# Optimization experiments

Measured on AMD Instinct MI355X. Metric: run time of the kernel, lower is better.

## Reference

```python
import jax, jax.numpy as jnp
import numpy as np

K = 3       # kernel_size
STRIDE = 1
PAD = 1
EPS = 1e-12  # F.normalize eps


def setup_inputs() -> dict:
    key = jax.random.key(0)
    k1, k2, k3 = jax.random.split(key, 3)
    x = jax.random.normal(k1, (8, 128, 112, 112), dtype=jnp.float32)
    weight = jax.random.normal(k2, (256, 128, K, K), dtype=jnp.float32)
    bias = jax.random.normal(k3, (256,), dtype=jnp.float32)
    return {"x": x, "weight": weight, "bias": bias}


def reference(x, weight, bias):
    B, C, H, W = x.shape
    Cout = weight.shape[0]
    oh = (H + 2 * PAD - K) // STRIDE + 1
    ow = (W + 2 * PAD - K) // STRIDE + 1
    # im2col: [B, C*K*K, oh, ow]; feature order (C, kh, kw), same as torch F.unfold
    patches = jax.lax.conv_general_dilated_patches(
        x, (K, K), (STRIDE, STRIDE), [(PAD, PAD), (PAD, PAD)],
        dimension_numbers=("NCHW", "OIHW", "NCHW"))
    u = patches.reshape(B, C * K * K, oh * ow)
    # L2-normalize each patch column (dim=1), matching F.normalize(p=2, dim=1)
    norm = jnp.sqrt(jnp.sum(u * u, axis=1, keepdims=True))
    u = u / jnp.maximum(norm, EPS)
    # GEMM: [Cout, C*K*K] x [B, C*K*K, L] -> [B, Cout, L]
    out = jnp.einsum("od,bdl->bol", weight.reshape(Cout, -1), u)
    out = out.reshape(B, Cout, oh, ow) + bias[None, :, None, None]
    return out
```

## Files before the change

### kernel.cpp

```cpp
#include <hip/hip_runtime.h>

#define CIN    128
#define COUT   256
#define Hh     112
#define Ww     112
#define HW     12544
#define NBATCH 8
#define NPIX   (NBATCH*HW)
#define KD     (CIN*9)
#define PH     114
#define PPIX   (NBATCH*PH*PH)

typedef __bf16         v8bf __attribute__((ext_vector_type(8)));
typedef float          v4f  __attribute__((ext_vector_type(4)));
typedef unsigned short v8us __attribute__((ext_vector_type(8)));

__device__ __forceinline__ unsigned short f2bf(float f) {
  unsigned int u = __float_as_uint(f);
  u += 0x7FFFu + ((u >> 16) & 1u);
  return (unsigned short)(u >> 16);
}

__device__ __forceinline__ void gl_lds16(const void* g, void* l) {
  __builtin_amdgcn_global_load_lds(
      (const __attribute__((address_space(1))) void*)g,
      (__attribute__((address_space(3))) void*)l, 16, 0, 0);
}

__global__ __launch_bounds__(256) void k_sq_convert(
    const float* __restrict__ x, unsigned short* __restrict__ xbp,
    float* __restrict__ sq2)
{
  int gid  = blockIdx.x * 256 + threadIdx.x;
  int half = gid >= NPIX ? 1 : 0;
  int p    = gid - half * NPIX;
  int b  = p / HW;
  int hw = p - b * HW;
  int oy = hw / Ww;
  int ox = hw - oy * Ww;
  const float* xp = x + (size_t)b * CIN * HW + hw + (size_t)half * 64 * HW;
  unsigned short* xo = xbp + ((size_t)(b * PH + oy + 1) * PH + (ox + 1)) * CIN + half * 64;
  float acc = 0.0f;
  for (int c0 = 0; c0 < 64; c0 += 8) {
    v8us buf;
#pragma unroll
    for (int j = 0; j < 8; ++j) {
      float v = xp[(size_t)(c0 + j) * HW];
      acc += v * v;
      buf[j] = f2bf(v);
    }
    *(v8us*)(xo + c0) = buf;
  }
  sq2[(size_t)half * NPIX + p] = acc;
}

__global__ __launch_bounds__(256) void k_zero_border(unsigned short* __restrict__ xbp)
{
  int gid = blockIdx.x * 256 + threadIdx.x;
  if (gid >= PPIX) return;
  int b  = gid / (PH * PH);
  int r  = gid - b * PH * PH;
  int py = r / PH;
  int px = r - py * PH;
  if (py != 0 && py != PH - 1 && px != 0 && px != PH - 1) return;
  unsigned short* dst = xbp + (size_t)gid * CIN;
  v8us z;
#pragma unroll
  for (int j = 0; j < 8; ++j) z[j] = 0;
#pragma unroll
  for (int c0 = 0; c0 < CIN; c0 += 8) *(v8us*)(dst + c0) = z;
}

__global__ __launch_bounds__(256) void k_invnorm(
    const float* __restrict__ sq2, float* __restrict__ invn)
{
  int p = blockIdx.x * 256 + threadIdx.x;
  if (p >= NPIX) return;
  int b  = p / HW;  int r  = p - b * HW;
  int oy = r / Ww;  int ox = r - oy * Ww;
  float acc = 0.0f;
#pragma unroll
  for (int dy = -1; dy <= 1; ++dy) {
    int iy = oy + dy;
    if (iy < 0 || iy >= Hh) continue;
#pragma unroll
    for (int dx = -1; dx <= 1; ++dx) {
      int ix = ox + dx;
      if (ix < 0 || ix >= Ww) continue;
      int q = b * HW + iy * Ww + ix;
      acc += sq2[q] + sq2[NPIX + q];
    }
  }
  invn[p] = 1.0f / fmaxf(sqrtf(acc), 1e-12f);
}

__global__ __launch_bounds__(256) void k_packw(
    const float* __restrict__ w, unsigned short* __restrict__ wp)
{
  int idx = blockIdx.x * 256 + threadIdx.x;
  int o  = idx / KD;
  int rr = idx - o * KD;
  int kk = rr >> 7;
  int c  = rr & 127;
  wp[idx] = f2bf(w[(size_t)o * KD + c * 9 + kk]);
}

__global__ __launch_bounds__(256, 3) void k_conv(
    const unsigned short* __restrict__ wp,
    const unsigned short* __restrict__ xbp,
    const float* __restrict__ invn,
    const float* __restrict__ bias,
    float* __restrict__ out)
{
  __shared__ unsigned short As[128 * 64];
  __shared__ unsigned short Bs[128 * 64];

  int tid  = threadIdx.x;
  int lane = tid & 63;
  int wid  = tid >> 6;
  int wm   = wid >> 1, wn = wid & 1;
  int quad = lane >> 4;
  int l16  = lane & 15;

  int bn = blockIdx.x;
  int bm = blockIdx.y;

  int srow = tid >> 3;
  int g    = (tid & 7) ^ (srow & 7);

  const unsigned short* asrc = wp + (size_t)(bm * 128 + srow) * KD + g * 8;

  int pb[4];
#pragma unroll
  for (int j = 0; j < 4; ++j) {
    int n  = bn * 128 + j * 32 + srow;
    int b  = n / HW;  int r  = n - b * HW;
    int oy = r / Ww;  int ox = r - oy * Ww;
    pb[j] = ((b * PH + oy) * PH + ox) * CIN + g * 8;
  }

  v4f acc[4][4];
#pragma unroll
  for (int mt = 0; mt < 4; ++mt)
#pragma unroll
    for (int nt = 0; nt < 4; ++nt)
#pragma unroll
      for (int j = 0; j < 4; ++j) acc[mt][nt][j] = 0.0f;

  const int khs[9] = {0,0,0,1,1,1,2,2,2};
  const int kws[9] = {0,1,2,0,1,2,0,1,2};

  for (int s = 0; s < 18; ++s) {
    int kk   = s >> 1;
    int c0   = (s & 1) * 64;
    int soff = (khs[kk] * PH + kws[kk]) * CIN + c0;

#pragma unroll
    for (int j = 0; j < 4; ++j)
      gl_lds16(asrc + (size_t)j * 32 * KD + s * 64,
               &As[(wid * 8 + j * 32) * 64]);
#pragma unroll
    for (int j = 0; j < 4; ++j)
      gl_lds16(xbp + pb[j] + soff,
               &Bs[(wid * 8 + j * 32) * 64]);

    __syncthreads();

#pragma unroll
    for (int h = 0; h < 2; ++h) {
      v8bf af[4], bf[4];
      int cch = (h * 4 + quad) ^ (l16 & 7);
#pragma unroll
      for (int mt = 0; mt < 4; ++mt) {
        int m = wm * 64 + mt * 16 + l16;
        af[mt] = *(const v8bf*)&As[m * 64 + cch * 8];
      }
#pragma unroll
      for (int nt = 0; nt < 4; ++nt) {
        int nr = wn * 64 + nt * 16 + l16;
        bf[nt] = *(const v8bf*)&Bs[nr * 64 + cch * 8];
      }
#pragma unroll
      for (int mt = 0; mt < 4; ++mt)
#pragma unroll
        for (int nt = 0; nt < 4; ++nt)
          acc[mt][nt] = __builtin_amdgcn_mfma_f32_16x16x32_bf16(
              af[mt], bf[nt], acc[mt][nt], 0, 0, 0);
    }

    __syncthreads();
  }

#pragma unroll
  for (int nt = 0; nt < 4; ++nt) {
    int n = bn * 128 + wn * 64 + nt * 16 + l16;
    float inv = invn[n];
    int b = n / HW;  int r = n - b * HW;
    float* op = out + (size_t)b * COUT * HW + r;
#pragma unroll
    for (int mt = 0; mt < 4; ++mt) {
      int o0 = bm * 128 + wm * 64 + mt * 16 + quad * 4;
#pragma unroll
      for (int reg = 0; reg < 4; ++reg) {
        int o = o0 + reg;
        op[(size_t)o * HW] = acc[mt][nt][reg] * inv + bias[o];
      }
    }
  }
}

extern "C" void kernel_launch(void* const* d_in, const int* in_sizes, int n_in,
                              void* d_out, int out_size, void* d_ws, size_t ws_size,
                              hipStream_t stream) {
  const float* x    = (const float*)d_in[0];
  const float* w    = (const float*)d_in[1];
  const float* bias = (const float*)d_in[2];
  float* out        = (float*)d_out;

  char* ws = (char*)d_ws;
  unsigned short* xbp = (unsigned short*)ws;
  size_t off = (size_t)PPIX * CIN * 2;
  unsigned short* wpk = (unsigned short*)(ws + off);
  off += (size_t)COUT * KD * 2;
  float* sq2 = (float*)(ws + off);
  off += (size_t)2 * NPIX * 4;
  float* invn = (float*)(ws + off);

  k_sq_convert<<<2 * NPIX / 256, 256, 0, stream>>>(x, xbp, sq2);
  k_zero_border<<<(PPIX + 255) / 256, 256, 0, stream>>>(xbp);
  k_packw<<<(COUT * KD) / 256, 256, 0, stream>>>(w, wpk);
  k_invnorm<<<NPIX / 256, 256, 0, stream>>>(sq2, invn);
  k_conv<<<dim3(NPIX / 128, COUT / 128), 256, 0, stream>>>(wpk, xbp, invn, bias, out);
}
```

Baseline: 244.4 us.

## Transpose input via LDS, stage conv epilogue through LDS, and swizzle block order

```diff
diff --git a/kernel.cpp b/kernel.cpp
--- a/kernel.cpp
+++ b/kernel.cpp
@@ -13,7 +13,6 @@
 
 typedef __bf16         v8bf __attribute__((ext_vector_type(8)));
 typedef float          v4f  __attribute__((ext_vector_type(4)));
-typedef unsigned short v8us __attribute__((ext_vector_type(8)));
 
 __device__ __forceinline__ unsigned short f2bf(float f) {
   unsigned int u = __float_as_uint(f);
@@ -27,31 +26,57 @@
       (__attribute__((address_space(3))) void*)l, 16, 0, 0);
 }
 
+#define SQS 65
 __global__ __launch_bounds__(256) void k_sq_convert(
     const float* __restrict__ x, unsigned short* __restrict__ xbp,
-    float* __restrict__ sq2)
-{
-  int gid  = blockIdx.x * 256 + threadIdx.x;
-  int half = gid >= NPIX ? 1 : 0;
-  int p    = gid - half * NPIX;
-  int b  = p / HW;
-  int hw = p - b * HW;
-  int oy = hw / Ww;
-  int ox = hw - oy * Ww;
-  const float* xp = x + (size_t)b * CIN * HW + hw + (size_t)half * 64 * HW;
-  unsigned short* xo = xbp + ((size_t)(b * PH + oy + 1) * PH + (ox + 1)) * CIN + half * 64;
+    float* __restrict__ sq)
+{
+  __shared__ unsigned int US[56 * SQS];
+  __shared__ float sqp[56 * 4];
+
+  int tid = threadIdx.x;
+  int l   = tid & 63;
+  int wid = tid >> 6;
+  int bid = blockIdx.x;
+  int xh  = bid & 1;
+  int t2  = bid >> 1;
+  int b   = t2 / Hh;
+  int oy  = t2 - b * Hh;
+  int ox0 = xh * 56;
+
+  const float* xp = x + (size_t)b * CIN * HW + oy * Ww + ox0;
+  bool valid = l < 56;
   float acc = 0.0f;
-  for (int c0 = 0; c0 < 64; c0 += 8) {
-    v8us buf;
-#pragma unroll
-    for (int j = 0; j < 8; ++j) {
-      float v = xp[(size_t)(c0 + j) * HW];
-      acc += v * v;
-      buf[j] = f2bf(v);
-    }
-    *(v8us*)(xo + c0) = buf;
-  }
-  sq2[(size_t)half * NPIX + p] = acc;
+#pragma unroll
+  for (int it = 0; it < 16; ++it) {
+    int cp = it * 4 + wid;
+    int c0 = cp * 2;
+    float v0 = 0.0f, v1 = 0.0f;
+    if (valid) {
+      v0 = xp[(size_t)c0 * HW + l];
+      v1 = xp[(size_t)(c0 + 1) * HW + l];
+    }
+    acc += v0 * v0 + v1 * v1;
+    unsigned int pk = (unsigned int)f2bf(v0) | ((unsigned int)f2bf(v1) << 16);
+    if (valid) US[l * SQS + cp] = pk;
+  }
+  if (valid) sqp[l * 4 + wid] = acc;
+  __syncthreads();
+
+  if (tid < 56) {
+    float s = sqp[tid * 4] + sqp[tid * 4 + 1] + sqp[tid * 4 + 2] + sqp[tid * 4 + 3];
+    sq[(size_t)b * HW + oy * Ww + ox0 + tid] = s;
+  }
+
+  unsigned int* dst = (unsigned int*)xbp +
+      ((size_t)(b * PH + oy + 1) * PH + (ox0 + 1)) * (CIN / 2);
+  for (int h = tid; h < 896; h += 256) {
+    int u0  = h * 4;
+    int pix = u0 >> 6, cu = u0 & 63;
+    const unsigned int* s = &US[pix * SQS + cu];
+    uint4 vv; vv.x = s[0]; vv.y = s[1]; vv.z = s[2]; vv.w = s[3];
+    *(uint4*)(dst + u0) = vv;
+  }
 }
 
 __global__ __launch_bounds__(256) void k_zero_border(unsigned short* __restrict__ xbp)
@@ -63,21 +88,20 @@
   int py = r / PH;
   int px = r - py * PH;
   if (py != 0 && py != PH - 1 && px != 0 && px != PH - 1) return;
-  unsigned short* dst = xbp + (size_t)gid * CIN;
-  v8us z;
-#pragma unroll
-  for (int j = 0; j < 8; ++j) z[j] = 0;
-#pragma unroll
-  for (int c0 = 0; c0 < CIN; c0 += 8) *(v8us*)(dst + c0) = z;
+  unsigned int* dst = (unsigned int*)xbp + (size_t)gid * (CIN / 2);
+  uint4 z = {0, 0, 0, 0};
+#pragma unroll
+  for (int c0 = 0; c0 < 64; c0 += 4) *(uint4*)(dst + c0) = z;
 }
 
 __global__ __launch_bounds__(256) void k_invnorm(
-    const float* __restrict__ sq2, float* __restrict__ invn)
+    const float* __restrict__ sq, float* __restrict__ invn)
 {
   int p = blockIdx.x * 256 + threadIdx.x;
   if (p >= NPIX) return;
   int b  = p / HW;  int r  = p - b * HW;
   int oy = r / Ww;  int ox = r - oy * Ww;
+  const float* s = sq + (size_t)b * HW;
   float acc = 0.0f;
 #pragma unroll
   for (int dy = -1; dy <= 1; ++dy) {
@@ -87,8 +111,7 @@
     for (int dx = -1; dx <= 1; ++dx) {
       int ix = ox + dx;
       if (ix < 0 || ix >= Ww) continue;
-      int q = b * HW + iy * Ww + ix;
-      acc += sq2[q] + sq2[NPIX + q];
+      acc += s[iy * Ww + ix];
     }
   }
   invn[p] = 1.0f / fmaxf(sqrtf(acc), 1e-12f);
@@ -105,6 +128,7 @@
   wp[idx] = f2bf(w[(size_t)o * KD + c * 9 + kk]);
 }
 
+#define SLAB_S 132
 __global__ __launch_bounds__(256, 3) void k_conv(
     const unsigned short* __restrict__ wp,
     const unsigned short* __restrict__ xbp,
@@ -112,8 +136,10 @@
     const float* __restrict__ bias,
     float* __restrict__ out)
 {
-  __shared__ unsigned short As[128 * 64];
-  __shared__ unsigned short Bs[128 * 64];
+  __shared__ __align__(16) char smem[64 * SLAB_S * 4];
+  unsigned short* As = (unsigned short*)smem;
+  unsigned short* Bs = As + 128 * 64;
+  float* slab = (float*)smem;
 
   int tid  = threadIdx.x;
   int lane = tid & 63;
@@ -122,21 +148,24 @@
   int quad = lane >> 4;
   int l16  = lane & 15;
 
-  int bn = blockIdx.x;
-  int bm = blockIdx.y;
+  int L  = blockIdx.x;
+  int g  = L >> 4;
+  int j  = L & 15;
+  int bn = g * 8 + (j & 7);
+  int bm = j >> 3;
 
   int srow = tid >> 3;
-  int g    = (tid & 7) ^ (srow & 7);
-
-  const unsigned short* asrc = wp + (size_t)(bm * 128 + srow) * KD + g * 8;
+  int g16  = (tid & 7) ^ (srow & 7);
+
+  const unsigned short* asrc = wp + (size_t)(bm * 128 + srow) * KD + g16 * 8;
 
   int pb[4];
 #pragma unroll
-  for (int j = 0; j < 4; ++j) {
-    int n  = bn * 128 + j * 32 + srow;
+  for (int jj = 0; jj < 4; ++jj) {
+    int n  = bn * 128 + jj * 32 + srow;
     int b  = n / HW;  int r  = n - b * HW;
     int oy = r / Ww;  int ox = r - oy * Ww;
-    pb[j] = ((b * PH + oy) * PH + ox) * CIN + g * 8;
+    pb[jj] = ((b * PH + oy) * PH + ox) * CIN + g16 * 8;
   }
 
   v4f acc[4][4];
@@ -145,7 +174,7 @@
 #pragma unroll
     for (int nt = 0; nt < 4; ++nt)
 #pragma unroll
-      for (int j = 0; j < 4; ++j) acc[mt][nt][j] = 0.0f;
+      for (int q = 0; q < 4; ++q) acc[mt][nt][q] = 0.0f;
 
   const int khs[9] = {0,0,0,1,1,1,2,2,2};
   const int kws[9] = {0,1,2,0,1,2,0,1,2};
@@ -156,13 +185,13 @@
     int soff = (khs[kk] * PH + kws[kk]) * CIN + c0;
 
 #pragma unroll
-    for (int j = 0; j < 4; ++j)
-      gl_lds16(asrc + (size_t)j * 32 * KD + s * 64,
-               &As[(wid * 8 + j * 32) * 64]);
-#pragma unroll
-    for (int j = 0; j < 4; ++j)
-      gl_lds16(xbp + pb[j] + soff,
-               &Bs[(wid * 8 + j * 32) * 64]);
+    for (int jj = 0; jj < 4; ++jj)
+      gl_lds16(asrc + (size_t)jj * 32 * KD + s * 64,
+               &As[(wid * 8 + jj * 32) * 64]);
+#pragma unroll
+    for (int jj = 0; jj < 4; ++jj)
+      gl_lds16(xbp + pb[jj] + soff,
+               &Bs[(wid * 8 + jj * 32) * 64]);
 
     __syncthreads();
 
@@ -171,15 +200,11 @@
       v8bf af[4], bf[4];
       int cch = (h * 4 + quad) ^ (l16 & 7);
 #pragma unroll
-      for (int mt = 0; mt < 4; ++mt) {
-        int m = wm * 64 + mt * 16 + l16;
-        af[mt] = *(const v8bf*)&As[m * 64 + cch * 8];
-      }
-#pragma unroll
-      for (int nt = 0; nt < 4; ++nt) {
-        int nr = wn * 64 + nt * 16 + l16;
-        bf[nt] = *(const v8bf*)&Bs[nr * 64 + cch * 8];
-      }
+      for (int mt = 0; mt < 4; ++mt)
+        af[mt] = *(const v8bf*)&As[(wm * 64 + mt * 16 + l16) * 64 + cch * 8];
+#pragma unroll
+      for (int nt = 0; nt < 4; ++nt)
+        bf[nt] = *(const v8bf*)&Bs[(wn * 64 + nt * 16 + l16) * 64 + cch * 8];
 #pragma unroll
       for (int mt = 0; mt < 4; ++mt)
 #pragma unroll
@@ -191,19 +216,45 @@
     __syncthreads();
   }
 
-#pragma unroll
-  for (int nt = 0; nt < 4; ++nt) {
-    int n = bn * 128 + wn * 64 + nt * 16 + l16;
-    float inv = invn[n];
-    int b = n / HW;  int r = n - b * HW;
-    float* op = out + (size_t)b * COUT * HW + r;
-#pragma unroll
-    for (int mt = 0; mt < 4; ++mt) {
-      int o0 = bm * 128 + wm * 64 + mt * 16 + quad * 4;
-#pragma unroll
-      for (int reg = 0; reg < 4; ++reg) {
-        int o = o0 + reg;
-        op[(size_t)o * HW] = acc[mt][nt][reg] * inv + bias[o];
+  int nbase = bn * 128;
+  int bb = nbase / HW;
+  int rr = nbase - bb * HW;
+  float* obase = out + (size_t)bb * COUT * HW + rr;
+
+  float invv[4];
+#pragma unroll
+  for (int nt = 0; nt < 4; ++nt)
+    invv[nt] = invn[nbase + wn * 64 + nt * 16 + l16];
+
+  for (int pass = 0; pass < 2; ++pass) {
+    if (pass) __syncthreads();
+    if (wm == pass) {
+#pragma unroll
+      for (int mt = 0; mt < 4; ++mt)
+#pragma unroll
+        for (int nt = 0; nt < 4; ++nt) {
+          int col = wn * 64 + nt * 16 + l16;
+#pragma unroll
+          for (int reg = 0; reg < 4; ++reg)
+            slab[(mt * 16 + quad * 4 + reg) * SLAB_S + col] =
+                acc[mt][nt][reg] * invv[nt];
+        }
+    }
+    __syncthreads();
+#pragma unroll
+    for (int it = 0; it < 2; ++it) {
+      int row = it * 32 + (tid >> 3);
+      int o   = bm * 128 + pass * 64 + row;
+      float bv = bias[o];
+      float* orow = obase + (size_t)o * HW;
+#pragma unroll
+      for (int k = 0; k < 4; ++k) {
+        int c4 = ((tid & 7) + k * 8) * 4;
+        v4f v = *(const v4f*)&slab[row * SLAB_S + c4];
+        v4f r2;
+#pragma unroll
+        for (int q = 0; q < 4; ++q) r2[q] = v[q] + bv;
+        *(v4f*)(orow + c4) = r2;
       }
     }
   }
@@ -222,13 +273,13 @@
   size_t off = (size_t)PPIX * CIN * 2;
   unsigned short* wpk = (unsigned short*)(ws + off);
   off += (size_t)COUT * KD * 2;
-  float* sq2 = (float*)(ws + off);
-  off += (size_t)2 * NPIX * 4;
+  float* sq = (float*)(ws + off);
+  off += (size_t)NPIX * 4;
   float* invn = (float*)(ws + off);
 
-  k_sq_convert<<<2 * NPIX / 256, 256, 0, stream>>>(x, xbp, sq2);
+  k_sq_convert<<<NBATCH * Hh * 2, 256, 0, stream>>>(x, xbp, sq);
   k_zero_border<<<(PPIX + 255) / 256, 256, 0, stream>>>(xbp);
   k_packw<<<(COUT * KD) / 256, 256, 0, stream>>>(w, wpk);
-  k_invnorm<<<NPIX / 256, 256, 0, stream>>>(sq2, invn);
-  k_conv<<<dim3(NPIX / 128, COUT / 128), 256, 0, stream>>>(wpk, xbp, invn, bias, out);
-}
+  k_invnorm<<<NPIX / 256, 256, 0, stream>>>(sq, invn);
+  k_conv<<<1568, 256, 0, stream>>>(wpk, xbp, invn, bias, out);
+}
```

New measurement: 216.2 us. -11.5%, faster.
